# Kernel optimization log

Measured on AMD Instinct MI355X. Metric: run time of the kernel, lower is better.

Reference implementation:

```python
import jax, jax.numpy as jnp
import numpy as np

# YOLOv1 loss constants (from init_kwargs)
S, B, C = 28, 2, 20
L_COORD, L_NOOBJ = 5.0, 0.5
LEN_PRED = 5 * B + C  # 30
BS = 512


def setup_inputs() -> dict:
    key = jax.random.key(0)
    k1, k2, k3 = jax.random.split(key, 3)
    prediction = jax.random.uniform(k1, (BS, S, S, LEN_PRED), dtype=jnp.float32)
    target = jax.random.uniform(k2, (BS, S, S, LEN_PRED), dtype=jnp.float32)
    obj = jax.random.bernoulli(k3, 0.05, (BS, S, S)).astype(jnp.float32)
    idx = jnp.arange(LEN_PRED)
    is_conf = (idx < 5 * B) & (idx % 5 == 4)
    target = jnp.where(is_conf, obj[..., None], target)
    return {"prediction": prediction, "target": target}


def _xyxy(box):
    # [x, y, w, h] (cell-relative center, image-relative wh) -> [x1, y1, x2, y2]
    xy = box[..., :2] / S
    wh = box[..., 2:4]
    return xy - 0.5 * wh, xy + 0.5 * wh


def reference(prediction, target):
    N = prediction.shape[0]
    dt = prediction.dtype
    coo = (target[..., 4] > 0).astype(dt)   # (bs,S,S) cells with an object
    noo = 1.0 - coo                          # cells without an object

    pb = prediction[..., :5 * B].reshape(prediction.shape[:3] + (B, 5))  # (bs,S,S,B,5)
    tb = target[..., :5 * B].reshape(target.shape[:3] + (B, 5))

    # IoU of each predicted box vs the (single) target box of the cell
    p_lt, p_rb = _xyxy(pb)                 # (bs,S,S,B,2)
    t_lt, t_rb = _xyxy(tb[..., 0, :])      # (bs,S,S,2)
    lt = jnp.maximum(p_lt, t_lt[..., None, :])
    rb = jnp.minimum(p_rb, t_rb[..., None, :])
    wh = jnp.clip(rb - lt, 0.0)
    inter = wh[..., 0] * wh[..., 1]        # (bs,S,S,B)
    area1 = jnp.prod(p_rb - p_lt, axis=-1)
    area2 = jnp.prod(t_rb - t_lt, axis=-1)[..., None]
    iou = jax.lax.stop_gradient(inter / (area1 + area2 - inter))  # .data in torch

    max_idx = jnp.argmax(iou, axis=-1)     # responsible box per cell
    max_iou = jnp.max(iou, axis=-1)
    resp = jax.nn.one_hot(max_idx, B, dtype=dt)    # (bs,S,S,B)
    w_resp = coo[..., None] * resp                  # responsible & object
    w_not = coo[..., None] * (1.0 - resp)           # not responsible & object

    # Term 1+2: location loss (xy MSE + sqrt-wh MSE) on responsible boxes
    d_xy = jnp.sum((pb[..., :2] - tb[..., :2]) ** 2, axis=-1)
    d_wh = jnp.sum((jnp.sqrt(pb[..., 2:4]) - jnp.sqrt(tb[..., 2:4])) ** 2, axis=-1)
    loc_loss = jnp.sum(w_resp * (d_xy + d_wh))

    contain_loss = jnp.sum(w_resp * (pb[..., 4] - max_iou[..., None]) ** 2)

    # Term 4a: not-responsible boxes in object cells -> confidence target 0
    not_response_loss = jnp.sum(w_not * pb[..., 4] ** 2)

    # Term 4b: confidence loss in no-object cells (all B boxes)
    nooobj_loss = jnp.sum(noo[..., None] * (pb[..., 4] - tb[..., 4]) ** 2)

    # Term 5: class MSE in object cells
    class_loss = jnp.sum(coo[..., None] * (prediction[..., 5 * B:] - target[..., 5 * B:]) ** 2)

    loss = (L_COORD * loc_loss + contain_loss
            + L_NOOBJ * (not_response_loss + nooobj_loss) + class_loss)
    return loss / N
```

## Files before the change

kernel.cpp:

```cpp
#include <hip/hip_runtime.h>

namespace {
constexpr int   kCells     = 512 * 28 * 28;
constexpr int   kHalfCells = 128;
constexpr int   kHalfF     = kHalfCells * 30;
constexpr int   kNHalves   = kCells / kHalfCells;
constexpr int   kNBlk      = 512;
constexpr int   kBaseH     = kNHalves / kNBlk;
constexpr int   kExtra     = kNHalves % kNBlk;
constexpr float kLCoord    = 5.0f;
constexpr float kLNoobj    = 0.5f;
constexpr float kInvS      = 1.0f / 28.0f;
constexpr float kInvN      = 1.0f / 512.0f;
}

__device__ __forceinline__ void async16(const float* g, float* l) {
    __builtin_amdgcn_global_load_lds(
        (const __attribute__((address_space(1))) void*)g,
        (__attribute__((address_space(3))) void*)l,
        16, 0, 0);
}
__device__ __forceinline__ void wait_vm15() { asm volatile("s_waitcnt vmcnt(15)" ::: "memory"); }
__device__ __forceinline__ void wait_vm0()  { asm volatile("s_waitcnt vmcnt(0)"  ::: "memory"); }

__device__ __forceinline__ float cell_loss(const float* p, const float* t) {
    const float coo = (t[4] > 0.0f) ? 1.0f : 0.0f;

    const float t_cx = t[0] * kInvS, t_cy = t[1] * kInvS;
    const float t_ltx = t_cx - 0.5f * t[2];
    const float t_lty = t_cy - 0.5f * t[3];
    const float t_rbx = t_cx + 0.5f * t[2];
    const float t_rby = t_cy + 0.5f * t[3];
    const float area2 = (t_rbx - t_ltx) * (t_rby - t_lty);

    float iou0 = 0.0f, iou1 = 0.0f;
    #pragma unroll
    for (int b = 0; b < 2; ++b) {
        const float* pb = p + 5 * b;
        const float p_cx = pb[0] * kInvS, p_cy = pb[1] * kInvS;
        const float p_ltx = p_cx - 0.5f * pb[2];
        const float p_lty = p_cy - 0.5f * pb[3];
        const float p_rbx = p_cx + 0.5f * pb[2];
        const float p_rby = p_cy + 0.5f * pb[3];
        const float ltx = fmaxf(p_ltx, t_ltx);
        const float lty = fmaxf(p_lty, t_lty);
        const float rbx = fminf(p_rbx, t_rbx);
        const float rby = fminf(p_rby, t_rby);
        const float w = fmaxf(rbx - ltx, 0.0f);
        const float h = fmaxf(rby - lty, 0.0f);
        const float inter = w * h;
        const float area1 = (p_rbx - p_ltx) * (p_rby - p_lty);
        const float iou = inter / (area1 + area2 - inter);
        if (b == 0) iou0 = iou; else iou1 = iou;
    }
    const int   max_idx = (iou1 > iou0) ? 1 : 0;
    const float max_iou = fmaxf(iou0, iou1);

    float loc = 0.0f, contain = 0.0f, notresp = 0.0f, nooobj = 0.0f;
    #pragma unroll
    for (int b = 0; b < 2; ++b) {
        const float* pb = p + 5 * b;
        const float* tb = t + 5 * b;
        const float dx = pb[0] - tb[0];
        const float dy = pb[1] - tb[1];
        const float d_xy = dx * dx + dy * dy;
        const float sw = sqrtf(pb[2]) - sqrtf(tb[2]);
        const float sh = sqrtf(pb[3]) - sqrtf(tb[3]);
        const float d_wh = sw * sw + sh * sh;
        const float resp   = (b == max_idx) ? 1.0f : 0.0f;
        const float w_resp = coo * resp;
        const float w_not  = coo * (1.0f - resp);
        loc += w_resp * (d_xy + d_wh);
        const float dc = pb[4] - max_iou;
        contain += w_resp * dc * dc;
        notresp += w_not * pb[4] * pb[4];
        const float dn = pb[4] - tb[4];
        nooobj += (1.0f - coo) * dn * dn;
    }

    float cls = 0.0f;
    #pragma unroll
    for (int j = 10; j < 30; ++j) {
        const float d = p[j] - t[j];
        cls += d * d;
    }
    cls *= coo;

    return kLCoord * loc + contain + kLNoobj * (notresp + nooobj) + cls;
}

template <bool USE_WS>
__global__ __launch_bounds__(128) void yolo_loss_kernel(
        const float* __restrict__ pred,
        const float* __restrict__ targ,
        float* __restrict__ dst) {
    __shared__ float lp[2][kHalfF];
    __shared__ float lt[2][kHalfF];
    __shared__ float wsum[2];

    const int tid  = threadIdx.x;
    const int lane = tid & 63;
    const int wid  = tid >> 6;
    const int b    = blockIdx.x;

    const int h0 = b * kBaseH + min(b, kExtra);
    const int H  = kBaseH + (b < kExtra ? 1 : 0);

    const float* gsrc = (wid == 0) ? pred : targ;

    auto stage = [&](int h, int buf) {
        const float* g = gsrc + (size_t)h * kHalfF;
        float* l = (wid == 0) ? &lp[buf][0] : &lt[buf][0];
        #pragma unroll
        for (int c = 0; c < 15; ++c) {
            const int f = c * 256 + lane * 4;
            async16(g + f, l + c * 256);
        }
    };

    stage(h0, 0);
    if (H > 1) stage(h0 + 1, 1);

    float acc = 0.0f;
    for (int i = 0; i < H; ++i) {
        const int buf = i & 1;
        if (i + 1 < H) wait_vm15(); else wait_vm0();
        __builtin_amdgcn_s_barrier();
        acc += cell_loss(&lp[buf][tid * 30], &lt[buf][tid * 30]);
        if (i + 2 < H) {
            __builtin_amdgcn_s_barrier();
            stage(h0 + i + 2, buf);
        }
    }

    #pragma unroll
    for (int off = 32; off > 0; off >>= 1)
        acc += __shfl_down(acc, off, 64);
    if (lane == 0) wsum[wid] = acc;
    __syncthreads();
    if (tid == 0) {
        const float s = wsum[0] + wsum[1];
        if (USE_WS) dst[b] = s;
        else        atomicAdd(dst, s * kInvN);
    }
}

__global__ __launch_bounds__(256) void reduce_kernel(
        const float* __restrict__ part, float* __restrict__ out) {
    __shared__ float wsum[4];
    float s = 0.0f;
    for (int i = threadIdx.x; i < kNBlk; i += 256) s += part[i];
    #pragma unroll
    for (int off = 32; off > 0; off >>= 1)
        s += __shfl_down(s, off, 64);
    const int lane = threadIdx.x & 63;
    const int wid  = threadIdx.x >> 6;
    if (lane == 0) wsum[wid] = s;
    __syncthreads();
    if (threadIdx.x == 0)
        out[0] = (wsum[0] + wsum[1] + wsum[2] + wsum[3]) * kInvN;
}

__global__ void zero_out_kernel(float* __restrict__ out) {
    if (threadIdx.x == 0) out[0] = 0.0f;
}

extern "C" void kernel_launch(void* const* d_in, const int* in_sizes, int n_in,
                              void* d_out, int out_size, void* d_ws, size_t ws_size,
                              hipStream_t stream) {
    const float* pred = (const float*)d_in[0];
    const float* targ = (const float*)d_in[1];
    float* out = (float*)d_out;

    if (ws_size >= (size_t)kNBlk * sizeof(float)) {
        float* part = (float*)d_ws;
        yolo_loss_kernel<true><<<kNBlk, 128, 0, stream>>>(pred, targ, part);
        reduce_kernel<<<1, 256, 0, stream>>>(part, out);
    } else {
        zero_out_kernel<<<1, 64, 0, stream>>>(out);
        yolo_loss_kernel<false><<<kNBlk, 128, 0, stream>>>(pred, targ, out);
    }
}
```

Baseline: 23.43 us.

## Replace async global-to-LDS copies with register-staged prefetch and larger tiles

Swaps the double-buffered global_load_lds pipeline for a single LDS buffer fed from registers: each thread loads 15 float4 of the next tile into registers while the current tile is computed, then stores them to LDS. The block grows to 256 threads with 256-cell tiles, and all waves share the load of both prediction and target. The aim is wider vector loads and fewer, larger tiles per block. The cost is 60 registers of prefetch per thread, an extra LDS store pass and two barriers per iteration, which can limit occupancy.

```diff
diff --git a/kernel.cpp b/kernel.cpp
--- a/kernel.cpp
+++ b/kernel.cpp
@@ -2,26 +2,19 @@
 
 namespace {
 constexpr int   kCells     = 512 * 28 * 28;
-constexpr int   kHalfCells = 128;
-constexpr int   kHalfF     = kHalfCells * 30;
-constexpr int   kNHalves   = kCells / kHalfCells;
+constexpr int   kTPB       = 256;
+constexpr int   kTileCells = 256;
+constexpr int   kTileF     = kTileCells * 30;
+constexpr int   kTileC4    = kTileF / 4;
+constexpr int   kNTiles    = kCells / kTileCells;
 constexpr int   kNBlk      = 512;
-constexpr int   kBaseH     = kNHalves / kNBlk;
-constexpr int   kExtra     = kNHalves % kNBlk;
+constexpr int   kBaseT     = kNTiles / kNBlk;
+constexpr int   kExtraT    = kNTiles % kNBlk;
 constexpr float kLCoord    = 5.0f;
 constexpr float kLNoobj    = 0.5f;
 constexpr float kInvS      = 1.0f / 28.0f;
 constexpr float kInvN      = 1.0f / 512.0f;
 }
-
-__device__ __forceinline__ void async16(const float* g, float* l) {
-    __builtin_amdgcn_global_load_lds(
-        (const __attribute__((address_space(1))) void*)g,
-        (__attribute__((address_space(3))) void*)l,
-        16, 0, 0);
-}
-__device__ __forceinline__ void wait_vm15() { asm volatile("s_waitcnt vmcnt(15)" ::: "memory"); }
-__device__ __forceinline__ void wait_vm0()  { asm volatile("s_waitcnt vmcnt(0)"  ::: "memory"); }
 
 __device__ __forceinline__ float cell_loss(const float* p, const float* t) {
     const float coo = (t[4] > 0.0f) ? 1.0f : 0.0f;
@@ -90,47 +83,53 @@
 }
 
 template <bool USE_WS>
-__global__ __launch_bounds__(128) void yolo_loss_kernel(
+__global__ __launch_bounds__(kTPB, 2) void yolo_loss_kernel(
         const float* __restrict__ pred,
         const float* __restrict__ targ,
         float* __restrict__ dst) {
-    __shared__ float lp[2][kHalfF];
-    __shared__ float lt[2][kHalfF];
-    __shared__ float wsum[2];
+    __shared__ float4 lds4[2 * kTileC4];
+    __shared__ float wsum[kTPB / 64];
 
     const int tid  = threadIdx.x;
     const int lane = tid & 63;
     const int wid  = tid >> 6;
     const int b    = blockIdx.x;
 
-    const int h0 = b * kBaseH + min(b, kExtra);
-    const int H  = kBaseH + (b < kExtra ? 1 : 0);
+    const int t0 = b * kBaseT + min(b, kExtraT);
+    const int H  = kBaseT + (b < kExtraT ? 1 : 0);
 
-    const float* gsrc = (wid == 0) ? pred : targ;
+    float* lds = reinterpret_cast<float*>(lds4);
 
-    auto stage = [&](int h, int buf) {
-        const float* g = gsrc + (size_t)h * kHalfF;
-        float* l = (wid == 0) ? &lp[buf][0] : &lt[buf][0];
+    float4 r[15];
+    auto issue = [&](int tile) {
+        const float* gp = pred + (size_t)tile * kTileF;
+        const float* gt = targ + (size_t)tile * kTileF;
         #pragma unroll
         for (int c = 0; c < 15; ++c) {
-            const int f = c * 256 + lane * 4;
-            async16(g + f, l + c * 256);
+            const int g = c * kTPB + tid;
+            const float* src = (g < kTileC4) ? (gp + (size_t)g * 4)
+                                             : (gt + (size_t)(g - kTileC4) * 4);
+            r[c] = *reinterpret_cast<const float4*>(src);
         }
     };
+    auto store = [&]() {
+        #pragma unroll
+        for (int c = 0; c < 15; ++c)
+            lds4[c * kTPB + tid] = r[c];
+    };
 
-    stage(h0, 0);
-    if (H > 1) stage(h0 + 1, 1);
-
+    issue(t0);
     float acc = 0.0f;
     for (int i = 0; i < H; ++i) {
-        const int buf = i & 1;
-        if (i + 1 < H) wait_vm15(); else wait_vm0();
+        if (i) {
+            asm volatile("s_waitcnt lgkmcnt(0)" ::: "memory");
+            __builtin_amdgcn_s_barrier();
+        }
+        store();
+        if (i + 1 < H) issue(t0 + i + 1);
+        asm volatile("s_waitcnt lgkmcnt(0)" ::: "memory");
         __builtin_amdgcn_s_barrier();
-        acc += cell_loss(&lp[buf][tid * 30], &lt[buf][tid * 30]);
-        if (i + 2 < H) {
-            __builtin_amdgcn_s_barrier();
-            stage(h0 + i + 2, buf);
-        }
+        acc += cell_loss(lds + tid * 30, lds + kTileF + tid * 30);
     }
 
     #pragma unroll
@@ -139,7 +138,7 @@
     if (lane == 0) wsum[wid] = acc;
     __syncthreads();
     if (tid == 0) {
-        const float s = wsum[0] + wsum[1];
+        const float s = wsum[0] + wsum[1] + wsum[2] + wsum[3];
         if (USE_WS) dst[b] = s;
         else        atomicAdd(dst, s * kInvN);
     }
@@ -174,10 +173,10 @@
 
     if (ws_size >= (size_t)kNBlk * sizeof(float)) {
         float* part = (float*)d_ws;
-        yolo_loss_kernel<true><<<kNBlk, 128, 0, stream>>>(pred, targ, part);
+        yolo_loss_kernel<true><<<kNBlk, kTPB, 0, stream>>>(pred, targ, part);
         reduce_kernel<<<1, 256, 0, stream>>>(part, out);
     } else {
         zero_out_kernel<<<1, 64, 0, stream>>>(out);
-        yolo_loss_kernel<false><<<kNBlk, 128, 0, stream>>>(pred, targ, out);
+        yolo_loss_kernel<false><<<kNBlk, kTPB, 0, stream>>>(pred, targ, out);
     }
 }
```

New measurement: 54.36 us. 2.32x slower.
